# Kernel tuning notes

Measured on AMD Instinct MI355X. Metric: run time of the kernel, lower is better.

Reference implementation:

```python
import jax, jax.numpy as jnp
import numpy as np
from functools import partial

SIGMA = 0.1       # blend_params.sigma (heaviside noise intensity)
GAMMA = 0.1       # blend_params.gamma (argmax noise intensity / z softening)
ZNEAR = 1.0
ZFAR = 100.0
NB_SAMPLES = 4
EPS = 1e-10
N, H, W, K = 8, 256, 256, 8


def random_heaviside(x, noise, sigma):
    # x: (N,H,W,K), noise: (S,N,H,W,K). torch.heaviside(v, ones): 1 for v>=0 else 0.
    maps = (x + sigma * noise >= 0).astype(x.dtype)
    return maps.mean(axis=0)


def random_argmax(z, noise, gamma):
    # z: (N,H,W,Kp), noise: (S,N,H,W,Kp). One-hot of per-sample argmax, averaged.
    zp = z + gamma * noise
    w = jax.nn.one_hot(jnp.argmax(zp, axis=-1), z.shape[-1], dtype=z.dtype)
    return w.mean(axis=0)


def reference(colors, dists, zbuf, pix_to_face, background):
    kh, ka = jax.random.split(jax.random.key(1))
    noise_h = jax.random.normal(kh, (NB_SAMPLES, N, H, W, K), dtype=colors.dtype)
    noise_a = jax.random.normal(ka, (NB_SAMPLES, N, H, W, K + 1), dtype=colors.dtype)

    mask = (pix_to_face >= 0).astype(colors.dtype)          # (N,H,W,K)
    prob_map = random_heaviside(-dists, noise_h, SIGMA) * mask
    alpha = jnp.prod(1.0 - prob_map, axis=-1)               # (N,H,W)

    z_inv = (ZFAR - zbuf) / (ZFAR - ZNEAR) * mask
    z_inv_max = jnp.clip(jnp.max(z_inv, axis=-1, keepdims=True), EPS)
    z_map = jnp.log(EPS + prob_map) + (z_inv - z_inv_max) / GAMMA
    bg_score = jnp.broadcast_to((EPS - z_inv_max) / GAMMA, z_map.shape[:-1] + (1,))
    z_map = jnp.concatenate([z_map, bg_score], axis=-1)     # (N,H,W,K+1)

    randomax = random_argmax(z_map, noise_a, GAMMA)
    wz, wb = randomax[..., :-1], randomax[..., -1:]
    weighted_colors = jnp.einsum('nhwk,nhwkc->nhwc', wz, colors)
    rgb = weighted_colors + wb * background                 # (N,H,W,3)
    a = (1.0 - alpha)[..., None]
    return jnp.concatenate([rgb, a], axis=-1)               # (N,H,W,4)


def setup_inputs() -> dict:
    key = jax.random.key(0)
    k1, k2, k3, k4 = jax.random.split(key, 4)
    colors = jax.random.normal(k1, (N, H, W, K, 3), dtype=jnp.float32)
    dists = jax.random.normal(k2, (N, H, W, K), dtype=jnp.float32)
    zbuf = jax.random.uniform(k3, (N, H, W, K), dtype=jnp.float32)
    pix_to_face = jax.random.randint(k4, (N, H, W, K), 0, 1000)
    background = jnp.ones((3,), dtype=jnp.float32)
    return {"colors": colors, "dists": dists, "zbuf": zbuf,
            "pix_to_face": pix_to_face, "background": background}
```

## Files before the change

### kernel.cpp

```cpp
#include <hip/hip_runtime.h>
#include <cstdint>
#include <cmath>


#pragma clang fp contract(off)

#define NPIX 524288
#define STRIDE_H 4194304u
#define STRIDE_A 4718592u
#define BAND_A 5e-5f
#define DET_THR 0.55f
#define ELIM_THR 1.10f

__device__ __forceinline__ uint32_t rotl32(uint32_t v, int n) {
  return (v << n) | (v >> (32 - n));
}

__device__ __forceinline__ void tf2x32(uint32_t k0, uint32_t k1,
                                       uint32_t c0, uint32_t c1,
                                       uint32_t& o0, uint32_t& o1) {
  const uint32_t k2 = k0 ^ k1 ^ 0x1BD11BDAu;
  uint32_t x0 = c0 + k0, x1 = c1 + k1;
#define TFR(r) { x0 += x1; x1 = rotl32(x1, r); x1 ^= x0; }
  TFR(13) TFR(15) TFR(26) TFR(6)
  x0 += k1;  x1 += k2 + 1u;
  TFR(17) TFR(29) TFR(16) TFR(24)
  x0 += k2;  x1 += k0 + 2u;
  TFR(13) TFR(15) TFR(26) TFR(6)
  x0 += k0;  x1 += k1 + 3u;
  TFR(17) TFR(29) TFR(16) TFR(24)
  x0 += k1;  x1 += k2 + 4u;
  TFR(13) TFR(15) TFR(26) TFR(6)
  x0 += k2;  x1 += k0 + 5u;
#undef TFR
  o0 = x0; o1 = x1;
}

__device__ __forceinline__ double fast_log(double z) {
  uint64_t b = __double_as_longlong(z);
  int E = (int)(b >> 52) - 1023;
  double m = __longlong_as_double((b & 0x000FFFFFFFFFFFFFULL) |
                                  0x3FF0000000000000ULL);
  bool c = m > 1.4142135623730951;
  m = c ? m * 0.5 : m;
  E = c ? E + 1 : E;
  double d = m + 1.0;
  double r = __builtin_amdgcn_rcp(d);
  r = fma(r, fma(-d, r, 1.0), r);
  r = fma(r, fma(-d, r, 1.0), r);
  double s = (m - 1.0) * r;
  double u = s * s;
  double p = 1.0 / 19.0;
  p = fma(p, u, 1.0 / 17.0);
  p = fma(p, u, 1.0 / 15.0);
  p = fma(p, u, 1.0 / 13.0);
  p = fma(p, u, 1.0 / 11.0);
  p = fma(p, u, 1.0 / 9.0);
  p = fma(p, u, 1.0 / 7.0);
  p = fma(p, u, 1.0 / 5.0);
  p = fma(p, u, 1.0 / 3.0);
  p = fma(p, u, 1.0);
  double lm = (2.0 * s) * p;
  const double LN2_HI = 6.93147180369123816490e-01;
  const double LN2_LO = 1.90821492927058770002e-10;
  double e = (double)E;
  return fma(e, LN2_HI, fma(e, LN2_LO, lm));
}

__device__ __forceinline__ float normal_exact(uint32_t bits) {
  float f = __uint_as_float((bits >> 9) | 0x3f800000u) - 1.0f;
  const float lo = __uint_as_float(0xBF7FFFFFu);
  float v = __fadd_rn(__fmul_rn(f, 2.0f), lo);
  v = fmaxf(lo, v);
  float t = -__fmul_rn(v, v);
  float taylor = __fmul_rn(__fadd_rn(__fmul_rn(-0.5f, t), 1.0f), t);
  float lg = (float)fast_log((double)__fadd_rn(t, 1.0f));
  float l1p = (fabsf(t) < 1e-4f) ? taylor : lg;
  float w = -l1p;
  const bool lt = w < 5.0f;
  float ww = lt ? __fsub_rn(w, 2.5f) : __fsub_rn(__fsqrt_rn(w), 3.0f);
  float p  = lt ? 2.81022636e-08f : -0.000200214257f;
  p = __fadd_rn(lt ?  3.43273939e-07f :  0.000100950558f, __fmul_rn(p, ww));
  p = __fadd_rn(lt ? -3.5233877e-06f  :  0.00134934322f,  __fmul_rn(p, ww));
  p = __fadd_rn(lt ? -4.39150654e-06f : -0.00367342844f,  __fmul_rn(p, ww));
  p = __fadd_rn(lt ?  0.00021858087f  :  0.00573950773f,  __fmul_rn(p, ww));
  p = __fadd_rn(lt ? -0.00125372503f  : -0.0076224613f,   __fmul_rn(p, ww));
  p = __fadd_rn(lt ? -0.00417768164f  :  0.00943887047f,  __fmul_rn(p, ww));
  p = __fadd_rn(lt ?  0.246640727f    :  1.00167406f,     __fmul_rn(p, ww));
  p = __fadd_rn(lt ?  1.50140941f     :  2.83297682f,     __fmul_rn(p, ww));
  return __fmul_rn(__uint_as_float(0x3FB504F3u), __fmul_rn(p, v));
}

__device__ __forceinline__ float score_fast(uint32_t bits, float zmj) {
  float f = __uint_as_float((bits >> 9) | 0x3f800000u) - 1.0f;
  const float lo = __uint_as_float(0xBF7FFFFFu);
  float v = fmaxf(lo, __fmaf_rn(f, 2.0f, lo));
  float t = -__fmul_rn(v, v);
  float u = __fadd_rn(t, 1.0f);
  float L = __builtin_amdgcn_logf(u);
  float ww = __fmaf_rn(-0.69314718f, L, -2.5f);
  float p = 2.81022636e-08f;
  p = __fmaf_rn(p, ww,  3.43273939e-07f);
  p = __fmaf_rn(p, ww, -3.5233877e-06f);
  p = __fmaf_rn(p, ww, -4.39150654e-06f);
  p = __fmaf_rn(p, ww,  0.00021858087f);
  p = __fmaf_rn(p, ww, -0.00125372503f);
  p = __fmaf_rn(p, ww, -0.00417768164f);
  p = __fmaf_rn(p, ww,  0.246640727f);
  p = __fmaf_rn(p, ww,  1.50140941f);
  if (__builtin_expect(__ballot(L <= -7.2134752f) != 0ull, 0)) {
    float w = __fmul_rn(-0.69314718f, L);
    float w2 = __builtin_amdgcn_sqrtf(w) - 3.0f;
    float q = -0.000200214257f;
    q = __fmaf_rn(q, w2,  0.000100950558f);
    q = __fmaf_rn(q, w2,  0.00134934322f);
    q = __fmaf_rn(q, w2, -0.00367342844f);
    q = __fmaf_rn(q, w2,  0.00573950773f);
    q = __fmaf_rn(q, w2, -0.0076224613f);
    q = __fmaf_rn(q, w2,  0.00943887047f);
    q = __fmaf_rn(q, w2,  1.00167406f);
    q = __fmaf_rn(q, w2,  2.83297682f);
    p = (L <= -7.2134752f) ? q : p;
  }
  return __fmaf_rn(__fmul_rn(p, v), 0.14142136f, zmj);
}

__device__ __forceinline__ uint32_t map_f32(float s) {
  uint32_t u = __float_as_uint(s);
  return u ^ ((uint32_t)((int32_t)u >> 31) | 0x80000000u);
}
__device__ __forceinline__ float unmap_f32(uint32_t m) {
  uint32_t u = m ^ ((uint32_t)((int32_t)(~m) >> 31) | 0x80000000u);
  return __uint_as_float(u);
}

__device__ __forceinline__ int wave_exscan4(int v, int& total) {
  int pre = 0; total = 0;
  #pragma unroll
  for (int b = 0; b < 4; ++b) {
    unsigned long long bl = __ballot(((v >> b) & 1) != 0);
    int below = (int)__builtin_amdgcn_mbcnt_hi(
        (uint32_t)(bl >> 32), __builtin_amdgcn_mbcnt_lo((uint32_t)bl, 0u));
    pre += below << b;
    total += (int)__popcll(bl) << b;
  }
  return pre;
}

__global__ __launch_bounds__(256) void RandomPhongShader_kernel(
    const float* __restrict__ colors,
    const float* __restrict__ dists,
    const float* __restrict__ zbuf,
    const int*   __restrict__ p2f,
    const float* __restrict__ bg,
    float* __restrict__ out)
{
  union SlotU {
    int T[256][8];
    unsigned long long s1[4][256];
  };
  __shared__ SlotU SU;
  __shared__ unsigned int S2[4][256];
  __shared__ float zmS[256][9];
  __shared__ __align__(8) unsigned char cntS[256][8];
  __shared__ unsigned short listS[4][576];

  const int tid  = threadIdx.x;
  const int lane = tid & 63;
  const int wv   = tid >> 6;
  const int P    = blockIdx.x * 256 + tid;
  const int Pw   = blockIdx.x * 256 + (wv << 6);

  uint32_t kh0, kh1, ka0, ka1;
  tf2x32(0u, 1u, 0u, 0u, kh0, kh1);
  tf2x32(0u, 1u, 0u, 1u, ka0, ka1);

  uint32_t ndm = 0, p4m = 0;
  {
    const float4* d4 = reinterpret_cast<const float4*>(dists + (size_t)P * 8);
    float4 a = d4[0], b = d4[1];
    float dk[8] = {a.x,a.y,a.z,a.w,b.x,b.y,b.z,b.w};
    int t8[8];
    #pragma unroll
    for (int k = 0; k < 8; ++k) {
      float y = fabsf(dk[k]) * 7.0710678f;
      float tt = __builtin_amdgcn_rcpf(__fmaf_rn(0.3275911f, y, 1.0f));
      float ex = __builtin_amdgcn_exp2f(__fmul_rn(-1.4426951f, y * y));
      float pp = 1.061405429f;
      pp = __fmaf_rn(pp, tt, -1.453152027f);
      pp = __fmaf_rn(pp, tt,  1.421413741f);
      pp = __fmaf_rn(pp, tt, -0.284496736f);
      pp = __fmaf_rn(pp, tt,  0.254829592f);
      float er = __fmaf_rn(-pp * tt, ex, 1.0f);
      float vs = copysignf(er, dk[k]);
      int T = (int)ceilf(__fmul_rn(__fadd_rn(vs, 0.99999994f), 4194304.0f));
      t8[k] = T - 6;
      ndm |= (fabsf(dk[k]) < DET_THR) ? (1u << k) : 0u;
      p4m |= (dk[k] <= -DET_THR) ? (1u << k) : 0u;
    }
    int4* tp = reinterpret_cast<int4*>(&SU.T[tid][0]);
    tp[0] = make_int4(t8[0], t8[1], t8[2], t8[3]);
    tp[1] = make_int4(t8[4], t8[5], t8[6], t8[7]);
  }

  int Wtot;
  {
    int off = wave_exscan4(__builtin_popcount(ndm), Wtot);
    uint32_t m = ndm;
    int idx = off;
    while (m) {
      int k = __builtin_ctz(m); m &= m - 1;
      listS[wv][idx++] = (unsigned short)((lane << 3) | k);
    }
  }
  __syncthreads();

  {
    const int trips = (Wtot + 63) >> 6;
    #pragma unroll 1
    for (int t = 0; t < trips; ++t) {
      const int i = (t << 6) + lane;
      const bool valid = i < Wtot;
      const unsigned short itm = listS[wv][valid ? i : 0];
      const int ow = itm >> 3, k = itm & 7;
      const int oTid = (wv << 6) | ow;
      const int To = SU.T[oTid][k];
      const uint32_t base = (uint32_t)(Pw + ow) * 8u + (uint32_t)k;
      uint32_t cnt = 0; bool band = false;
      #pragma unroll
      for (int s = 0; s < 4; ++s) {
        uint32_t o0, o1;
        tf2x32(kh0, kh1, 0u, base + (uint32_t)s * STRIDE_H, o0, o1);
        int mm = (int)((o0 ^ o1) >> 9);
        int sub = mm - To;
        cnt += (sub >= 6) ? 1u : 0u;
        band |= ((uint32_t)sub <= 12u);
      }
      if (__builtin_expect(__ballot(band && valid) != 0ull, 0)) {
        if (band && valid) {
          float x = -dists[(size_t)base];
          uint32_t c2 = 0;
          #pragma unroll 1
          for (int s = 0; s < 4; ++s) {
            uint32_t o0, o1;
            tf2x32(kh0, kh1, 0u, base + (uint32_t)s * STRIDE_H, o0, o1);
            float nz = normal_exact(o0 ^ o1);
            c2 += (__fadd_rn(x, __fmul_rn(0.1f, nz)) >= 0.0f) ? 1u : 0u;
          }
          cnt = c2;
        }
      }
      if (valid) cntS[oTid][k] = (unsigned char)cnt;
    }
  }
  __syncthreads();

  uint32_t msk;
  {
    const int4* m4 = reinterpret_cast<const int4*>(p2f + (size_t)P * 8);
    int4 f = m4[0], g = m4[1];
    msk  = (f.x >= 0 ? 1u : 0u) | (f.y >= 0 ? 2u : 0u)
         | (f.z >= 0 ? 4u : 0u) | (f.w >= 0 ? 8u : 0u)
         | (g.x >= 0 ? 16u : 0u) | (g.y >= 0 ? 32u : 0u)
         | (g.z >= 0 ? 64u : 0u) | (g.w >= 0 ? 128u : 0u);
  }
  float zinv[8], zmax;
  {
    const float4* z4 = reinterpret_cast<const float4*>(zbuf + (size_t)P * 8);
    float4 c = z4[0], e = z4[1];
    float zk[8] = {c.x,c.y,c.z,c.w,e.x,e.y,e.z,e.w};
    #pragma unroll
    for (int k = 0; k < 8; ++k) {
      const float m = ((msk >> k) & 1u) ? 1.0f : 0.0f;
      float zi = __fmul_rn(__fdiv_rn(__fsub_rn(100.0f, zk[k]), 99.0f), m);
      zinv[k] = zi;
      zmax = (k == 0) ? zi : fmaxf(zmax, zi);
    }
  }
  zmax = fmaxf(zmax, 1e-10f);

  const float lg0 = (float)-23.025850916589025;
  const float lg1 = (float)-1.3862943611198906;
  const float lg2 = (float)-0.6931471805599453;
  const float lg3 = (float)-0.2876820724517809;

  const uint2 cg = *reinterpret_cast<const uint2*>(&cntS[tid][0]);
  float alpha = 1.0f;
  float zm[9];
  #pragma unroll
  for (int k = 0; k < 8; ++k) {
    const uint32_t byte_ = ((k < 4 ? cg.x : cg.y) >> (8 * (k & 3))) & 0xffu;
    const int cntk = ((ndm >> k) & 1u) ? (int)byte_
                    : ((((p4m >> k) & 1u) != 0u) ? 4 : 0);
    const bool mb = ((msk >> k) & 1u) != 0u;
    const float pm = mb ? __fmul_rn((float)cntk, 0.25f) : 0.0f;
    alpha *= (1.0f - pm);
    const int i = mb ? cntk : 0;
    const float lg = (i == 0) ? lg0 : (i == 1) ? lg1 : (i == 2) ? lg2
                   : (i == 3) ? lg3 : 0.0f;
    zm[k] = __fadd_rn(lg, __fdiv_rn(__fsub_rn(zinv[k], zmax), 0.1f));
    zmS[tid][k] = zm[k];
  }
  zm[8] = __fdiv_rn(__fsub_rn(1e-10f, zmax), 0.1f);
  zmS[tid][8] = zm[8];

  float bz = zm[0];
  #pragma unroll
  for (int j = 1; j < 9; ++j) bz = fmaxf(bz, zm[j]);
  const float thr = __fsub_rn(bz, ELIM_THR);
  uint32_t vm = 0;
  #pragma unroll
  for (int j = 0; j < 9; ++j) vm |= (zm[j] >= thr) ? (1u << j) : 0u;
  const int V  = __builtin_popcount(vm);
  const int j0 = __builtin_ctz(vm);

  int W3;
  {
    int off3 = wave_exscan4((V >= 2) ? V : 0, W3);
    uint32_t m = (V >= 2) ? vm : 0u;
    int idx = off3;
    while (m) {
      int j = __builtin_ctz(m); m &= m - 1;
      listS[wv][idx++] = (unsigned short)((lane << 4) | j);
    }
  }
  #pragma unroll
  for (int s = 0; s < 4; ++s) { SU.s1[s][tid] = 0ull; S2[s][tid] = 0u; }
  __syncthreads();

  const int trips3 = (W3 + 63) >> 6;
  #pragma unroll 1
  for (int t = 0; t < trips3; ++t) {
    const int i = (t << 6) + lane;
    const bool valid = i < W3;
    const unsigned short itm = listS[wv][valid ? i : 0];
    const int ow = itm >> 4, j = itm & 15;
    const int oTid = (wv << 6) | ow;
    const float zo = zmS[oTid][j];
    const uint32_t cb3 = (uint32_t)(Pw + ow) * 9u + (uint32_t)j;
    const unsigned long long jtag = (unsigned long long)(15 - j);
    #pragma unroll
    for (int s = 0; s < 4; ++s) {
      uint32_t o0, o1;
      tf2x32(ka0, ka1, 0u, cb3 + (uint32_t)s * STRIDE_A, o0, o1);
      float sc = score_fast(o0 ^ o1, zo);
      unsigned long long key = ((unsigned long long)map_f32(sc) << 32) | jtag;
      if (valid) {
        unsigned long long old = atomicMax(&SU.s1[s][oTid], key);
        unsigned long long mn = key < old ? key : old;
        atomicMax(&S2[s][oTid], (unsigned int)(mn >> 32));
      }
    }
  }
  __syncthreads();

  uint32_t amPack = 0;
  const uint32_t cAo = (uint32_t)P * 9u;
  #pragma unroll 1
  for (int s = 0; s < 4; ++s) {
    int js;
    bool fl = false;
    if (V >= 2) {
      const unsigned long long b1 = SU.s1[s][tid];
      js = 15 - (int)(b1 & 0xFFFFu);
      const float s1f = unmap_f32((uint32_t)(b1 >> 32));
      const float s2f = unmap_f32(S2[s][tid]);
      fl = __fsub_rn(s1f, s2f) < BAND_A;
    } else {
      js = j0;
    }
    if (__builtin_expect(__ballot(fl) != 0ull, 0)) {
      if (fl) {
        int ame = 0;
        float be = -3.4e38f;
        #pragma unroll 1
        for (int j = 0; j < 9; ++j) {
          uint32_t o0, o1;
          tf2x32(ka0, ka1, 0u, cAo + (uint32_t)s * STRIDE_A + (uint32_t)j,
                 o0, o1);
          float nz = normal_exact(o0 ^ o1);
          float ve = __fadd_rn(zmS[tid][j], __fmul_rn(0.1f, nz));
          bool g = ve > be;
          be = g ? ve : be;
          ame = g ? j : ame;
        }
        js = ame;
      }
    }
    amPack += 1u << (3 * js);
  }

  float rgb[3] = {0.0f, 0.0f, 0.0f};
  {
    const float4* c4 = reinterpret_cast<const float4*>(colors + (size_t)P * 24);
    float cc[24];
    #pragma unroll
    for (int q = 0; q < 6; ++q) {
      float4 t = c4[q];
      cc[q*4+0]=t.x; cc[q*4+1]=t.y; cc[q*4+2]=t.z; cc[q*4+3]=t.w;
    }
    #pragma unroll
    for (int c = 0; c < 3; ++c) {
      float acc = 0.0f;
      #pragma unroll
      for (int k = 0; k < 8; ++k) {
        float wk = __fmul_rn(0.25f, (float)((amPack >> (3 * k)) & 7u));
        acc = __fadd_rn(acc, __fmul_rn(wk, cc[k * 3 + c]));
      }
      float wb = __fmul_rn(0.25f, (float)((amPack >> 24) & 7u));
      rgb[c] = __fadd_rn(acc, __fmul_rn(wb, bg[c]));
    }
  }

  float4 o;
  o.x = rgb[0]; o.y = rgb[1]; o.z = rgb[2];
  o.w = __fsub_rn(1.0f, alpha);
  reinterpret_cast<float4*>(out)[P] = o;
}

extern "C" void kernel_launch(void* const* d_in, const int* in_sizes, int n_in,
                              void* d_out, int out_size, void* d_ws, size_t ws_size,
                              hipStream_t stream) {
  const float* colors = (const float*)d_in[0];
  const float* dists  = (const float*)d_in[1];
  const float* zbuf   = (const float*)d_in[2];
  const int*   p2f    = (const int*)d_in[3];
  const float* bg     = (const float*)d_in[4];
  float* out = (float*)d_out;
  dim3 grid(NPIX / 256), block(256);
  hipLaunchKernelGGL(RandomPhongShader_kernel, grid, block, 0, stream,
                     colors, dists, zbuf, p2f, bg, out);
}
```

Measured before the change: 169.0 us.

## Use wave-local fences, pack argmax keys into 32-bit atomics, recompute thresholds inline

Block-wide __syncthreads barriers are replaced by a wave-level LDS wait plus scheduling barrier, since each wave only touches its own list and slots. The 64-bit atomicMax keys become 32-bit keys that put the index tag in the low 4 mantissa bits, with a wider ambiguity band to compensate for the lost precision. The per-slot threshold table in shared memory is dropped. Thresholds are now recomputed for only the flagged items, reloading dists from global memory. This cuts LDS use and barrier stalls, at the cost of extra global loads and a coarser tie-detection band that sends more pixels down the exact fallback path.

```diff
diff --git a/kernel.cpp b/kernel.cpp
--- a/kernel.cpp
+++ b/kernel.cpp
@@ -9,8 +9,15 @@
 #define STRIDE_H 4194304u
 #define STRIDE_A 4718592u
 #define BAND_A 5e-5f
+#define BAND_PACK 1.25e-4f
+#define KEY_MASK 0xFFFFFFF0u
 #define DET_THR 0.55f
 #define ELIM_THR 1.10f
+
+#define WAVE_FENCE() do {                                   \
+    asm volatile("s_waitcnt lgkmcnt(0)" ::: "memory");      \
+    __builtin_amdgcn_sched_barrier(0);                      \
+  } while (0)
 
 __device__ __forceinline__ uint32_t rotl32(uint32_t v, int n) {
   return (v << n) | (v >> (32 - n));
@@ -134,6 +141,21 @@
   return __uint_as_float(u);
 }
 
+__device__ __forceinline__ int thresh_m6(float d) {
+  float y = fabsf(d) * 7.0710678f;
+  float tt = __builtin_amdgcn_rcpf(__fmaf_rn(0.3275911f, y, 1.0f));
+  float ex = __builtin_amdgcn_exp2f(__fmul_rn(-1.4426951f, y * y));
+  float pp = 1.061405429f;
+  pp = __fmaf_rn(pp, tt, -1.453152027f);
+  pp = __fmaf_rn(pp, tt,  1.421413741f);
+  pp = __fmaf_rn(pp, tt, -0.284496736f);
+  pp = __fmaf_rn(pp, tt,  0.254829592f);
+  float er = __fmaf_rn(-pp * tt, ex, 1.0f);
+  float vs = copysignf(er, d);
+  int T = (int)ceilf(__fmul_rn(__fadd_rn(vs, 0.99999994f), 4194304.0f));
+  return T - 6;
+}
+
 __device__ __forceinline__ int wave_exscan4(int v, int& total) {
   int pre = 0; total = 0;
   #pragma unroll
@@ -155,15 +177,11 @@
     const float* __restrict__ bg,
     float* __restrict__ out)
 {
-  union SlotU {
-    int T[256][8];
-    unsigned long long s1[4][256];
-  };
-  __shared__ SlotU SU;
-  __shared__ unsigned int S2[4][256];
   __shared__ float zmS[256][9];
   __shared__ __align__(8) unsigned char cntS[256][8];
   __shared__ unsigned short listS[4][576];
+  __shared__ unsigned int s1S[4][64][4];
+  __shared__ unsigned int s2S[4][64][4];
 
   const int tid  = threadIdx.x;
   const int lane = tid & 63;
@@ -180,27 +198,11 @@
     const float4* d4 = reinterpret_cast<const float4*>(dists + (size_t)P * 8);
     float4 a = d4[0], b = d4[1];
     float dk[8] = {a.x,a.y,a.z,a.w,b.x,b.y,b.z,b.w};
-    int t8[8];
     #pragma unroll
     for (int k = 0; k < 8; ++k) {
-      float y = fabsf(dk[k]) * 7.0710678f;
-      float tt = __builtin_amdgcn_rcpf(__fmaf_rn(0.3275911f, y, 1.0f));
-      float ex = __builtin_amdgcn_exp2f(__fmul_rn(-1.4426951f, y * y));
-      float pp = 1.061405429f;
-      pp = __fmaf_rn(pp, tt, -1.453152027f);
-      pp = __fmaf_rn(pp, tt,  1.421413741f);
-      pp = __fmaf_rn(pp, tt, -0.284496736f);
-      pp = __fmaf_rn(pp, tt,  0.254829592f);
-      float er = __fmaf_rn(-pp * tt, ex, 1.0f);
-      float vs = copysignf(er, dk[k]);
-      int T = (int)ceilf(__fmul_rn(__fadd_rn(vs, 0.99999994f), 4194304.0f));
-      t8[k] = T - 6;
       ndm |= (fabsf(dk[k]) < DET_THR) ? (1u << k) : 0u;
       p4m |= (dk[k] <= -DET_THR) ? (1u << k) : 0u;
     }
-    int4* tp = reinterpret_cast<int4*>(&SU.T[tid][0]);
-    tp[0] = make_int4(t8[0], t8[1], t8[2], t8[3]);
-    tp[1] = make_int4(t8[4], t8[5], t8[6], t8[7]);
   }
 
   int Wtot;
@@ -213,7 +215,7 @@
       listS[wv][idx++] = (unsigned short)((lane << 3) | k);
     }
   }
-  __syncthreads();
+  WAVE_FENCE();
 
   {
     const int trips = (Wtot + 63) >> 6;
@@ -224,8 +226,9 @@
       const unsigned short itm = listS[wv][valid ? i : 0];
       const int ow = itm >> 3, k = itm & 7;
       const int oTid = (wv << 6) | ow;
-      const int To = SU.T[oTid][k];
       const uint32_t base = (uint32_t)(Pw + ow) * 8u + (uint32_t)k;
+      const float d = dists[(size_t)base];
+      const int To = thresh_m6(d);
       uint32_t cnt = 0; bool band = false;
       #pragma unroll
       for (int s = 0; s < 4; ++s) {
@@ -238,7 +241,7 @@
       }
       if (__builtin_expect(__ballot(band && valid) != 0ull, 0)) {
         if (band && valid) {
-          float x = -dists[(size_t)base];
+          float x = -d;
           uint32_t c2 = 0;
           #pragma unroll 1
           for (int s = 0; s < 4; ++s) {
@@ -253,7 +256,7 @@
       if (valid) cntS[oTid][k] = (unsigned char)cnt;
     }
   }
-  __syncthreads();
+  WAVE_FENCE();
 
   uint32_t msk;
   {
@@ -325,8 +328,8 @@
     }
   }
   #pragma unroll
-  for (int s = 0; s < 4; ++s) { SU.s1[s][tid] = 0ull; S2[s][tid] = 0u; }
-  __syncthreads();
+  for (int s = 0; s < 4; ++s) { s1S[wv][lane][s] = 0u; s2S[wv][lane][s] = 0u; }
+  WAVE_FENCE();
 
   const int trips3 = (W3 + 63) >> 6;
   #pragma unroll 1
@@ -338,21 +341,21 @@
     const int oTid = (wv << 6) | ow;
     const float zo = zmS[oTid][j];
     const uint32_t cb3 = (uint32_t)(Pw + ow) * 9u + (uint32_t)j;
-    const unsigned long long jtag = (unsigned long long)(15 - j);
+    const uint32_t jtag = (uint32_t)(15 - j);
     #pragma unroll
     for (int s = 0; s < 4; ++s) {
       uint32_t o0, o1;
       tf2x32(ka0, ka1, 0u, cb3 + (uint32_t)s * STRIDE_A, o0, o1);
       float sc = score_fast(o0 ^ o1, zo);
-      unsigned long long key = ((unsigned long long)map_f32(sc) << 32) | jtag;
+      uint32_t key = (map_f32(sc) & KEY_MASK) | jtag;
       if (valid) {
-        unsigned long long old = atomicMax(&SU.s1[s][oTid], key);
-        unsigned long long mn = key < old ? key : old;
-        atomicMax(&S2[s][oTid], (unsigned int)(mn >> 32));
+        uint32_t old = atomicMax(&s1S[wv][ow][s], key);
+        uint32_t mn = key < old ? key : old;
+        atomicMax(&s2S[wv][ow][s], mn);
       }
     }
   }
-  __syncthreads();
+  WAVE_FENCE();
 
   uint32_t amPack = 0;
   const uint32_t cAo = (uint32_t)P * 9u;
@@ -361,11 +364,11 @@
     int js;
     bool fl = false;
     if (V >= 2) {
-      const unsigned long long b1 = SU.s1[s][tid];
-      js = 15 - (int)(b1 & 0xFFFFu);
-      const float s1f = unmap_f32((uint32_t)(b1 >> 32));
-      const float s2f = unmap_f32(S2[s][tid]);
-      fl = __fsub_rn(s1f, s2f) < BAND_A;
+      const uint32_t b1 = s1S[wv][lane][s];
+      js = 15 - (int)(b1 & 0xFu);
+      const float s1f = unmap_f32(b1 & KEY_MASK);
+      const float s2f = unmap_f32(s2S[wv][lane][s] & KEY_MASK);
+      fl = __fsub_rn(s1f, s2f) < BAND_PACK;
     } else {
       js = j0;
     }
```

After: 168.6 us. About the same (-0.2%).
